# Kernel optimization log

Hardware: AMD Instinct MI355X
Metric: run time of the kernel (lower is better)

The kernel has to match this reference:

```python
import jax, jax.numpy as jnp
import numpy as np

D_MODEL = 1024
NUM_HEADS = 16
D_K = 64
D_V = 64


def setup_inputs() -> dict:
    key = jax.random.key(0)
    ks = jax.random.split(key, 9)
    s = 1.0 / np.sqrt(D_MODEL)
    inp = {
        "x": jax.random.normal(ks[0], (4, 2048, D_MODEL), dtype=jnp.float32),
        "Wq": jax.random.uniform(ks[1], (D_MODEL, NUM_HEADS * D_K), jnp.float32, -s, s),
        "bq": jnp.zeros((NUM_HEADS * D_K,), jnp.float32),
        "Wk": jax.random.uniform(ks[2], (D_MODEL, NUM_HEADS * D_K), jnp.float32, -s, s),
        "bk": jnp.zeros((NUM_HEADS * D_K,), jnp.float32),
        "Wv": jax.random.uniform(ks[3], (D_MODEL, NUM_HEADS * D_V), jnp.float32, -s, s),
        "bv": jnp.zeros((NUM_HEADS * D_V,), jnp.float32),
        "Wo": jax.random.uniform(ks[4], (NUM_HEADS * D_V, D_MODEL), jnp.float32, -s, s),
        "bo": jnp.zeros((D_MODEL,), jnp.float32),
        "gamma": jnp.ones((D_MODEL,), jnp.float32),
        "beta": jnp.zeros((D_MODEL,), jnp.float32),
    }
    return inp


def _layer_norm(x, gamma, beta, eps=1e-5):
    mu = jnp.mean(x, axis=-1, keepdims=True)
    var = jnp.var(x, axis=-1, keepdims=True)
    return (x - mu) * jax.lax.rsqrt(var + eps) * gamma + beta


def reference(x, Wq, bq, Wk, bk, Wv, bv, Wo, bo, gamma, beta):
    B, S, _ = x.shape
    residual = x
    xn = _layer_norm(x, gamma, beta)
    # projections -> [B, H, S, d]
    q = (xn @ Wq + bq).reshape(B, S, NUM_HEADS, D_K).transpose(0, 2, 1, 3)
    k = (xn @ Wk + bk).reshape(B, S, NUM_HEADS, D_K).transpose(0, 2, 1, 3)
    v = (xn @ Wv + bv).reshape(B, S, NUM_HEADS, D_V).transpose(0, 2, 1, 3)
    scores = jnp.einsum("bhqd,bhkd->bhqk", q, k) / jnp.sqrt(jnp.float32(D_K))
    causal = jnp.tril(jnp.ones((S, S), dtype=bool))  # [S, S]
    scores = jnp.where(causal, scores, -jnp.inf)
    attn = jax.nn.softmax(scores, axis=-1)
    out = jnp.einsum("bhqk,bhkd->bhqd", attn, v)  # [B, H, S, d_v]
    out = out.transpose(0, 2, 1, 3).reshape(B, S, NUM_HEADS * D_V)
    out = out @ Wo + bo
    return out + residual  # dropout p=0.0 -> identity
```

## Files before the change

### kernel.cpp

```cpp
#include <hip/hip_runtime.h>
#include <hip/hip_bf16.h>

#define D_MODEL 1024
#define NHEADS 16
#define DK 64
#define SEQ 2048
#define BATCH 4
#define M_TOTAL (BATCH * SEQ)
#define N_QKV (3 * D_MODEL)

#define QSCALE 0.1803368801111f

typedef __attribute__((ext_vector_type(8))) short short8;
typedef __attribute__((ext_vector_type(4))) float f32x4;
typedef __attribute__((ext_vector_type(16))) float f32x16;

typedef const __attribute__((address_space(1))) unsigned int* gas_p;
typedef __attribute__((address_space(3))) unsigned int* las_p;

__device__ __forceinline__ void gl_lds16(const void* g, void* l) {
    __builtin_amdgcn_global_load_lds((gas_p)g, (las_p)l, 16, 0, 0);
}

__device__ __forceinline__ f32x4 mfma16(short8 a, short8 b, f32x4 c) {
    return __builtin_amdgcn_mfma_f32_16x16x32_bf16(a, b, c, 0, 0, 0);
}

__device__ __forceinline__ f32x16 mfma32(short8 a, short8 b, f32x16 c) {
    return __builtin_amdgcn_mfma_f32_32x32x16_bf16(a, b, c, 0, 0, 0);
}

__device__ __forceinline__ unsigned short f2bf(float f) {
    union { float f; unsigned int u; } v; v.f = f;
    unsigned int r = v.u + 0x7fffu + ((v.u >> 16) & 1u);
    return (unsigned short)(r >> 16);
}

__device__ __forceinline__ unsigned int cvtpk(float lo, float hi) {
    unsigned int r;
    asm("v_cvt_pk_bf16_f32 %0, %1, %2" : "=v"(r) : "v"(lo), "v"(hi));
    return r;
}
__device__ __forceinline__ void plswap(unsigned int& a, unsigned int& b) {
    asm("v_permlane32_swap_b32 %0, %1" : "+v"(a), "+v"(b));
}

__global__ __launch_bounds__(256) void ln_kernel(const float* __restrict__ x,
                                                 const float* __restrict__ gamma,
                                                 const float* __restrict__ beta,
                                                 unsigned short* __restrict__ xn) {
    int row = blockIdx.x;
    int tid = threadIdx.x;
    const float4* xr = (const float4*)(x + (size_t)row * D_MODEL);
    float4 v = xr[tid];
    float s  = v.x + v.y + v.z + v.w;
    float ss = v.x * v.x + v.y * v.y + v.z * v.z + v.w * v.w;
    for (int off = 32; off > 0; off >>= 1) {
        s  += __shfl_down(s, off, 64);
        ss += __shfl_down(ss, off, 64);
    }
    __shared__ float red[8];
    int wid = tid >> 6;
    if ((tid & 63) == 0) { red[wid] = s; red[wid + 4] = ss; }
    __syncthreads();
    float st  = red[0] + red[1] + red[2] + red[3];
    float sst = red[4] + red[5] + red[6] + red[7];
    float mu  = st * (1.0f / D_MODEL);
    float var = sst * (1.0f / D_MODEL) - mu * mu;
    float rs  = rsqrtf(var + 1e-5f);
    const float4* g4 = (const float4*)gamma;
    const float4* b4 = (const float4*)beta;
    float4 g = g4[tid], b = b4[tid];
    ushort4 o;
    o.x = f2bf((v.x - mu) * rs * g.x + b.x);
    o.y = f2bf((v.y - mu) * rs * g.y + b.y);
    o.z = f2bf((v.z - mu) * rs * g.z + b.z);
    o.w = f2bf((v.w - mu) * rs * g.w + b.w);
    *(ushort4*)(xn + (size_t)row * D_MODEL + tid * 4) = o;
}

__global__ __launch_bounds__(256) void transpose_cast(const float* __restrict__ src,
                                                      unsigned short* __restrict__ dst,
                                                      int K, int N) {
    __shared__ unsigned short tile[32][33];
    int n0 = blockIdx.x * 32;
    int k0 = blockIdx.y * 32;
    int tx = threadIdx.x;
    int ty = threadIdx.y;
    for (int i = 0; i < 4; i++) {
        int k = k0 + ty + i * 8;
        tile[ty + i * 8][tx] = f2bf(src[(size_t)k * N + n0 + tx]);
    }
    __syncthreads();
    for (int i = 0; i < 4; i++) {
        int n = n0 + ty + i * 8;
        dst[(size_t)n * K + k0 + tx] = tile[tx][ty + i * 8];
    }
}

__global__ void bias_concat(const float* __restrict__ bq, const float* __restrict__ bk,
                            const float* __restrict__ bv, float* __restrict__ cat) {
    int i = blockIdx.x * 256 + threadIdx.x;
    if (i < N_QKV)
        cat[i] = (i < 1024) ? bq[i] : (i < 2048 ? bk[i - 1024] : bv[i - 2048]);
}

__global__ __launch_bounds__(256) void transpose_v(const unsigned short* __restrict__ qkv,
                                                   unsigned short* __restrict__ vt) {
    __shared__ __align__(16) unsigned short tile[64 * 72];
    int s0 = blockIdx.x * 64;
    int bh = blockIdx.y;
    int b = bh >> 4, h = bh & 15;
    int tid = threadIdx.x;
    const unsigned short* src = qkv + (size_t)(b * SEQ + s0) * N_QKV + 2048 + h * DK;
    for (int it = 0; it < 2; it++) {
        int o = tid + it * 256;
        int sl = o >> 3, ck = o & 7;
        short8 v = *(const short8*)(src + (size_t)sl * N_QKV + ck * 8);
        *(short8*)&tile[sl * 72 + ((ck ^ ((sl >> 3) & 7)) * 8)] = v;
    }
    __syncthreads();
    unsigned short* dst = vt + (size_t)bh * DK * SEQ + s0;
    for (int it = 0; it < 2; it++) {
        int o = tid + it * 256;
        int d = o >> 3, sc = (o & 7) * 8;
        short8 v;
        for (int i = 0; i < 8; i++)
            ((unsigned short*)&v)[i] =
                tile[(sc + i) * 72 + (((d >> 3) ^ (o & 7)) * 8) + (d & 7)];
        *(short8*)(dst + (size_t)d * SEQ + sc) = v;
    }
}

template <int MODE>
__global__ __launch_bounds__(256) void gemm128(const unsigned short* __restrict__ A,
                                               const unsigned short* __restrict__ Bt,
                                               const float* __restrict__ bias,
                                               const float* __restrict__ residual,
                                               void* __restrict__ Cout,
                                               int M, int N, int K) {
    constexpr int BM = 128, BN = 128, BK = 32;
    __shared__ __align__(16) unsigned short As[BM * BK];
    __shared__ __align__(16) unsigned short Bs[BN * BK];
    int m0 = blockIdx.y * BM;
    int n0 = blockIdx.x * BN;
    int tid = threadIdx.x;
    int wave = tid >> 6, lane = tid & 63;
    int wm = wave >> 1, wn = wave & 1;
    f32x4 acc[4][4] = {};

    int srow = wave * 32 + (lane >> 2);
    int scol = (lane & 3) * 8;
    const unsigned short* Ag0 = A + (size_t)(m0 + srow) * K + scol;
    const unsigned short* Ag1 = A + (size_t)(m0 + srow + 16) * K + scol;
    const unsigned short* Bg0 = Bt + (size_t)(n0 + srow) * K + scol;
    const unsigned short* Bg1 = Bt + (size_t)(n0 + srow + 16) * K + scol;
    unsigned short* Al0 = &As[(wave * 32) * BK];
    unsigned short* Al1 = &As[(wave * 32 + 16) * BK];
    unsigned short* Bl0 = &Bs[(wave * 32) * BK];
    unsigned short* Bl1 = &Bs[(wave * 32 + 16) * BK];

    int fr = lane & 15;
    int fq = lane >> 4;
    for (int k0 = 0; k0 < K; k0 += BK) {
        gl_lds16(Ag0 + k0, Al0);
        gl_lds16(Ag1 + k0, Al1);
        gl_lds16(Bg0 + k0, Bl0);
        gl_lds16(Bg1 + k0, Bl1);
        __syncthreads();
        short8 a[4], b[4];
        for (int ms = 0; ms < 4; ms++)
            a[ms] = *(short8*)&As[(wm * 64 + ms * 16 + fr) * BK + fq * 8];
        for (int ns = 0; ns < 4; ns++)
            b[ns] = *(short8*)&Bs[(wn * 64 + ns * 16 + fr) * BK + fq * 8];
        for (int ms = 0; ms < 4; ms++)
            for (int ns = 0; ns < 4; ns++)
                acc[ms][ns] = mfma16(a[ms], b[ns], acc[ms][ns]);
        __syncthreads();
    }
    for (int ms = 0; ms < 4; ms++)
        for (int ns = 0; ns < 4; ns++)
            for (int i = 0; i < 4; i++) {
                int r = m0 + wm * 64 + ms * 16 + fq * 4 + i;
                int c = n0 + wn * 64 + ns * 16 + fr;
                float val = acc[ms][ns][i] + bias[c];
                if (MODE == 0) {
                    if (c < D_MODEL) val *= QSCALE;
                    ((unsigned short*)Cout)[(size_t)r * N + c] = f2bf(val);
                } else {
                    ((float*)Cout)[(size_t)r * N + c] = val + residual[(size_t)r * N + c];
                }
            }
}

__global__ __launch_bounds__(256, 4) void attn_kernel(const unsigned short* __restrict__ qkv,
                                                      const unsigned short* __restrict__ vt,
                                                      unsigned short* __restrict__ attn_out) {
    __shared__ __align__(16) unsigned short Ks[2][64 * 64];
    __shared__ __align__(16) unsigned short Vs[2][64 * 64];
    constexpr int NSTRIP = SEQ / 128;
    int n = blockIdx.x;
    int qs = NSTRIP - 1 - (n >> 6);
    int bh = n & 63;
    int b = bh >> 4, h = bh & 15;
    int tid = threadIdx.x, w = tid >> 6, lane = tid & 63;
    int l5 = lane >> 5;
    int q31 = lane & 31;
    int l7 = lane & 7;
    int S0 = qs * 128;
    int qg = S0 + w * 32 + q31;
    int jmax = 2 * qs + 1;
    int jd = 2 * qs + (w >> 1);

    const unsigned short* kbase = qkv + (size_t)(b * SEQ) * N_QKV + D_MODEL + h * DK;
    const unsigned short* vtb = vt + (size_t)bh * DK * SEQ;

    const unsigned short* qptr = qkv + (size_t)(b * SEQ + qg) * N_QKV + h * DK;
    short8 qf[4];
#pragma unroll
    for (int s = 0; s < 4; s++)
        qf[s] = *(const short8*)(qptr + 16 * s + 8 * l5);

    int srow = lane >> 3;
    int schunk = (l7 ^ srow) * 8;

    f32x16 ot0 = {}, ot1 = {};
    float mold = -1e30f, lsum = 0.f;

#pragma unroll
    for (int c = 0; c < 2; c++) {
        int rl_ = w * 16 + c * 8;
        gl_lds16(kbase + (size_t)(rl_ + srow) * N_QKV + schunk, &Ks[0][rl_ * 64]);
        gl_lds16(vtb + (size_t)(rl_ + srow) * SEQ + schunk, &Vs[0][rl_ * 64]);
    }
    __syncthreads();

    for (int j = 0; j <= jmax; j++) {
        int bb = j & 1;
        if (j < jmax) {
#pragma unroll
            for (int c = 0; c < 2; c++) {
                int rl_ = w * 16 + c * 8;
                gl_lds16(kbase + (size_t)((j + 1) * 64 + rl_ + srow) * N_QKV + schunk,
                         &Ks[bb ^ 1][rl_ * 64]);
                gl_lds16(vtb + (size_t)(rl_ + srow) * SEQ + (j + 1) * 64 + schunk,
                         &Vs[bb ^ 1][rl_ * 64]);
            }
        }
        if (j <= jd) {
            const unsigned short* kb = Ks[bb];
            const unsigned short* vb = Vs[bb];
            f32x16 s0 = {}, s1 = {};
            __builtin_amdgcn_s_setprio(1);
#pragma unroll
            for (int s = 0; s < 4; s++) {
                int co = (((s << 1) | l5) ^ l7) * 8;
                short8 k0 = *(const short8*)&kb[(q31) * 64 + co];
                short8 k1 = *(const short8*)&kb[(32 + q31) * 64 + co];
                s0 = mfma32(k0, qf[s], s0);
                s1 = mfma32(k1, qf[s], s1);
            }
            __builtin_amdgcn_s_setprio(0);
            if (j == jd) {
#pragma unroll
                for (int r = 0; r < 16; r++) {
                    int kv0 = j * 64 + (r & 3) + 8 * (r >> 2) + 4 * l5;
                    if (kv0 > qg) s0[r] = -1e30f;
                    if (kv0 + 32 > qg) s1[r] = -1e30f;
                }
            }
            float tm[16];
#pragma unroll
            for (int r = 0; r < 16; r++) tm[r] = fmaxf(s0[r], s1[r]);
#pragma unroll
            for (int st = 8; st > 0; st >>= 1)
#pragma unroll
                for (int r = 0; r < 8; r++)
                    if (r < st) tm[r] = fmaxf(tm[r], tm[r + st]);
            float mloc = fmaxf(tm[0], __shfl_xor(tm[0], 32));
            if (!__all(mloc - mold <= 11.0f)) {
                float mnew = fmaxf(mold, mloc);
                float aexp = exp2f(mold - mnew);
                lsum *= aexp;
#pragma unroll
                for (int r = 0; r < 16; r++) { ot0[r] *= aexp; ot1[r] *= aexp; }
                mold = mnew;
            }
            float ts[16];
#pragma unroll
            for (int r = 0; r < 16; r++) {
                s0[r] = exp2f(s0[r] - mold);
                s1[r] = exp2f(s1[r] - mold);
                ts[r] = s0[r] + s1[r];
            }
#pragma unroll
            for (int st = 8; st > 0; st >>= 1)
#pragma unroll
                for (int r = 0; r < 8; r++)
                    if (r < st) ts[r] += ts[r + st];
            lsum += ts[0] + __shfl_xor(ts[0], 32);

            union { unsigned int wd[4]; short8 v; } pf;
#pragma unroll
            for (int t = 0; t < 4; t++) {
                int b2 = t & 1;
                unsigned int pa, pb, pc, pd;
                if (t < 2) {
                    pa = cvtpk(s0[8 * b2 + 0], s0[8 * b2 + 1]);
                    pb = cvtpk(s0[8 * b2 + 2], s0[8 * b2 + 3]);
                    pc = cvtpk(s0[8 * b2 + 4], s0[8 * b2 + 5]);
                    pd = cvtpk(s0[8 * b2 + 6], s0[8 * b2 + 7]);
                } else {
                    pa = cvtpk(s1[8 * b2 + 0], s1[8 * b2 + 1]);
                    pb = cvtpk(s1[8 * b2 + 2], s1[8 * b2 + 3]);
                    pc = cvtpk(s1[8 * b2 + 4], s1[8 * b2 + 5]);
                    pd = cvtpk(s1[8 * b2 + 6], s1[8 * b2 + 7]);
                }
                plswap(pa, pc);
                plswap(pb, pd);
                pf.wd[0] = pa; pf.wd[1] = pb; pf.wd[2] = pc; pf.wd[3] = pd;
                int co = (((t << 1) | l5) ^ l7) * 8;
                short8 v0 = *(const short8*)&vb[(q31) * 64 + co];
                short8 v1 = *(const short8*)&vb[(32 + q31) * 64 + co];
                __builtin_amdgcn_s_setprio(1);
                ot0 = mfma32(v0, pf.v, ot0);
                ot1 = mfma32(v1, pf.v, ot1);
                __builtin_amdgcn_s_setprio(0);
            }
        }
        __syncthreads();
    }

    float rl = 1.0f / lsum;
    unsigned short* ob = attn_out + (size_t)(b * SEQ + qg) * D_MODEL + h * DK + 4 * l5;
#pragma unroll
    for (int qq = 0; qq < 4; qq++) {
        uint2 val;
        val.x = cvtpk(ot0[4 * qq + 0] * rl, ot0[4 * qq + 1] * rl);
        val.y = cvtpk(ot0[4 * qq + 2] * rl, ot0[4 * qq + 3] * rl);
        *(uint2*)(ob + 8 * qq) = val;
        val.x = cvtpk(ot1[4 * qq + 0] * rl, ot1[4 * qq + 1] * rl);
        val.y = cvtpk(ot1[4 * qq + 2] * rl, ot1[4 * qq + 3] * rl);
        *(uint2*)(ob + 32 + 8 * qq) = val;
    }
}

extern "C" void kernel_launch(void* const* d_in, const int* in_sizes, int n_in,
                              void* d_out, int out_size, void* d_ws, size_t ws_size,
                              hipStream_t stream) {
    const float* x     = (const float*)d_in[0];
    const float* Wq    = (const float*)d_in[1];
    const float* bq    = (const float*)d_in[2];
    const float* Wk    = (const float*)d_in[3];
    const float* bk    = (const float*)d_in[4];
    const float* Wv    = (const float*)d_in[5];
    const float* bv    = (const float*)d_in[6];
    const float* Wo    = (const float*)d_in[7];
    const float* bo    = (const float*)d_in[8];
    const float* gamma = (const float*)d_in[9];
    const float* beta  = (const float*)d_in[10];
    float* out = (float*)d_out;

    char* ws = (char*)d_ws;
    unsigned short* xn     = (unsigned short*)ws;
    unsigned short* aout   = xn;
    unsigned short* wqkv_t = (unsigned short*)(ws + (16u << 20));
    unsigned short* wo_t   = (unsigned short*)(ws + (22u << 20));
    unsigned short* qkv    = (unsigned short*)(ws + (24u << 20));
    unsigned short* vt     = (unsigned short*)(ws + (72u << 20));
    float* biascat         = (float*)(ws + (88u << 20));

    ln_kernel<<<M_TOTAL, 256, 0, stream>>>(x, gamma, beta, xn);
    dim3 tb(32, 8);
    transpose_cast<<<dim3(32, 32), tb, 0, stream>>>(Wq, wqkv_t, 1024, 1024);
    transpose_cast<<<dim3(32, 32), tb, 0, stream>>>(Wk, wqkv_t + 1024 * 1024, 1024, 1024);
    transpose_cast<<<dim3(32, 32), tb, 0, stream>>>(Wv, wqkv_t + 2 * 1024 * 1024, 1024, 1024);
    transpose_cast<<<dim3(32, 32), tb, 0, stream>>>(Wo, wo_t, 1024, 1024);
    bias_concat<<<12, 256, 0, stream>>>(bq, bk, bv, biascat);

    gemm128<0><<<dim3(N_QKV / 128, M_TOTAL / 128), 256, 0, stream>>>(
        xn, wqkv_t, biascat, nullptr, qkv, M_TOTAL, N_QKV, D_MODEL);

    transpose_v<<<dim3(SEQ / 64, BATCH * NHEADS), 256, 0, stream>>>(qkv, vt);

    attn_kernel<<<dim3((SEQ / 128) * BATCH * NHEADS), 256, 0, stream>>>(qkv, vt, aout);

    gemm128<1><<<dim3(D_MODEL / 128, M_TOTAL / 128), 256, 0, stream>>>(
        aout, wo_t, bo, x, out, M_TOTAL, D_MODEL, D_MODEL);
}
```

Baseline: 303.0 us.

## Double-buffer GEMM LDS loads, remap workgroups across XCDs, merge weight prep kernels

The GEMM main loop now double-buffers its shared-memory tiles, issuing global-to-LDS loads for the next K step before computing on the current one, with explicit vmcnt waits and barriers. Workgroup IDs are remapped so consecutive tiles land on the same XCD, which should improve L2 reuse. The four weight transpose launches and the bias concat are merged into one kernel to cut launch overhead. The cost is twice the LDS per block, which may lower occupancy.

```diff
diff --git a/kernel.cpp b/kernel.cpp
--- a/kernel.cpp
+++ b/kernel.cpp
@@ -79,30 +79,41 @@
     *(ushort4*)(xn + (size_t)row * D_MODEL + tid * 4) = o;
 }
 
-__global__ __launch_bounds__(256) void transpose_cast(const float* __restrict__ src,
-                                                      unsigned short* __restrict__ dst,
-                                                      int K, int N) {
+__global__ __launch_bounds__(256) void prep_weights(const float* __restrict__ Wq,
+                                                    const float* __restrict__ Wk,
+                                                    const float* __restrict__ Wv,
+                                                    const float* __restrict__ Wo,
+                                                    const float* __restrict__ bq,
+                                                    const float* __restrict__ bk,
+                                                    const float* __restrict__ bv,
+                                                    unsigned short* __restrict__ wqkv_t,
+                                                    unsigned short* __restrict__ wo_t,
+                                                    float* __restrict__ biascat) {
     __shared__ unsigned short tile[32][33];
+    int z = blockIdx.z;
+    const float* src = (z == 0) ? Wq : (z == 1) ? Wk : (z == 2) ? Wv : Wo;
+    unsigned short* dst = (z == 0) ? wqkv_t
+                        : (z == 1) ? wqkv_t + 1024 * 1024
+                        : (z == 2) ? wqkv_t + 2 * 1024 * 1024
+                                   : wo_t;
     int n0 = blockIdx.x * 32;
     int k0 = blockIdx.y * 32;
     int tx = threadIdx.x;
     int ty = threadIdx.y;
     for (int i = 0; i < 4; i++) {
         int k = k0 + ty + i * 8;
-        tile[ty + i * 8][tx] = f2bf(src[(size_t)k * N + n0 + tx]);
+        tile[ty + i * 8][tx] = f2bf(src[(size_t)k * 1024 + n0 + tx]);
     }
     __syncthreads();
     for (int i = 0; i < 4; i++) {
         int n = n0 + ty + i * 8;
-        dst[(size_t)n * K + k0 + tx] = tile[tx][ty + i * 8];
-    }
-}
-
-__global__ void bias_concat(const float* __restrict__ bq, const float* __restrict__ bk,
-                            const float* __restrict__ bv, float* __restrict__ cat) {
-    int i = blockIdx.x * 256 + threadIdx.x;
-    if (i < N_QKV)
-        cat[i] = (i < 1024) ? bq[i] : (i < 2048 ? bk[i - 1024] : bv[i - 2048]);
+        dst[(size_t)n * 1024 + k0 + tx] = tile[tx][ty + i * 8];
+    }
+    if (z == 3 && blockIdx.x == 0 && blockIdx.y == 0) {
+        int tid = ty * 32 + tx;
+        for (int i = tid; i < N_QKV; i += 256)
+            biascat[i] = (i < 1024) ? bq[i] : (i < 2048 ? bk[i - 1024] : bv[i - 2048]);
+    }
 }
 
 __global__ __launch_bounds__(256) void transpose_v(const unsigned short* __restrict__ qkv,
@@ -140,10 +151,16 @@
                                                void* __restrict__ Cout,
                                                int M, int N, int K) {
     constexpr int BM = 128, BN = 128, BK = 32;
-    __shared__ __align__(16) unsigned short As[BM * BK];
-    __shared__ __align__(16) unsigned short Bs[BN * BK];
-    int m0 = blockIdx.y * BM;
-    int n0 = blockIdx.x * BN;
+    __shared__ __align__(16) unsigned short As[2][BM * BK];
+    __shared__ __align__(16) unsigned short Bs[2][BN * BK];
+    int nbx = gridDim.x;
+    int nwg = nbx * gridDim.y;
+    int orig = blockIdx.y * nbx + blockIdx.x;
+    int qq_ = nwg >> 3;
+    int wg = (orig & 7) * qq_ + (orig >> 3);
+    int m0 = (wg / nbx) * BM;
+    int n0 = (wg % nbx) * BN;
+
     int tid = threadIdx.x;
     int wave = tid >> 6, lane = tid & 63;
     int wm = wave >> 1, wn = wave & 1;
@@ -155,28 +172,38 @@
     const unsigned short* Ag1 = A + (size_t)(m0 + srow + 16) * K + scol;
     const unsigned short* Bg0 = Bt + (size_t)(n0 + srow) * K + scol;
     const unsigned short* Bg1 = Bt + (size_t)(n0 + srow + 16) * K + scol;
-    unsigned short* Al0 = &As[(wave * 32) * BK];
-    unsigned short* Al1 = &As[(wave * 32 + 16) * BK];
-    unsigned short* Bl0 = &Bs[(wave * 32) * BK];
-    unsigned short* Bl1 = &Bs[(wave * 32 + 16) * BK];
 
     int fr = lane & 15;
     int fq = lane >> 4;
-    for (int k0 = 0; k0 < K; k0 += BK) {
-        gl_lds16(Ag0 + k0, Al0);
-        gl_lds16(Ag1 + k0, Al1);
-        gl_lds16(Bg0 + k0, Bl0);
-        gl_lds16(Bg1 + k0, Bl1);
-        __syncthreads();
+    const int T = K / BK;
+
+    gl_lds16(Ag0, &As[0][(wave * 32) * BK]);
+    gl_lds16(Ag1, &As[0][(wave * 32 + 16) * BK]);
+    gl_lds16(Bg0, &Bs[0][(wave * 32) * BK]);
+    gl_lds16(Bg1, &Bs[0][(wave * 32 + 16) * BK]);
+
+    for (int t = 0; t < T; t++) {
+        int cur = t & 1;
+        if (t + 1 < T) {
+            int nk = (t + 1) * BK;
+            gl_lds16(Ag0 + nk, &As[cur ^ 1][(wave * 32) * BK]);
+            gl_lds16(Ag1 + nk, &As[cur ^ 1][(wave * 32 + 16) * BK]);
+            gl_lds16(Bg0 + nk, &Bs[cur ^ 1][(wave * 32) * BK]);
+            gl_lds16(Bg1 + nk, &Bs[cur ^ 1][(wave * 32 + 16) * BK]);
+            asm volatile("s_waitcnt vmcnt(4)" ::: "memory");
+        } else {
+            asm volatile("s_waitcnt vmcnt(0)" ::: "memory");
+        }
+        asm volatile("s_barrier" ::: "memory");
         short8 a[4], b[4];
         for (int ms = 0; ms < 4; ms++)
-            a[ms] = *(short8*)&As[(wm * 64 + ms * 16 + fr) * BK + fq * 8];
+            a[ms] = *(short8*)&As[cur][(wm * 64 + ms * 16 + fr) * BK + fq * 8];
         for (int ns = 0; ns < 4; ns++)
-            b[ns] = *(short8*)&Bs[(wn * 64 + ns * 16 + fr) * BK + fq * 8];
+            b[ns] = *(short8*)&Bs[cur][(wn * 64 + ns * 16 + fr) * BK + fq * 8];
         for (int ms = 0; ms < 4; ms++)
             for (int ns = 0; ns < 4; ns++)
                 acc[ms][ns] = mfma16(a[ms], b[ns], acc[ms][ns]);
-        __syncthreads();
+        asm volatile("s_barrier" ::: "memory");
     }
     for (int ms = 0; ms < 4; ms++)
         for (int ns = 0; ns < 4; ns++)
@@ -371,12 +398,8 @@
     float* biascat         = (float*)(ws + (88u << 20));
 
     ln_kernel<<<M_TOTAL, 256, 0, stream>>>(x, gamma, beta, xn);
-    dim3 tb(32, 8);
-    transpose_cast<<<dim3(32, 32), tb, 0, stream>>>(Wq, wqkv_t, 1024, 1024);
-    transpose_cast<<<dim3(32, 32), tb, 0, stream>>>(Wk, wqkv_t + 1024 * 1024, 1024, 1024);
-    transpose_cast<<<dim3(32, 32), tb, 0, stream>>>(Wv, wqkv_t + 2 * 1024 * 1024, 1024, 1024);
-    transpose_cast<<<dim3(32, 32), tb, 0, stream>>>(Wo, wo_t, 1024, 1024);
-    bias_concat<<<12, 256, 0, stream>>>(bq, bk, bv, biascat);
+    prep_weights<<<dim3(32, 32, 4), dim3(32, 8), 0, stream>>>(
+        Wq, Wk, Wv, Wo, bq, bk, bv, wqkv_t, wo_t, biascat);
 
     gemm128<0><<<dim3(N_QKV / 128, M_TOTAL / 128), 256, 0, stream>>>(
         xn, wqkv_t, biascat, nullptr, qkv, M_TOTAL, N_QKV, D_MODEL);
```

Measured after the change: 283.7 us. 1.07x faster.
